# Optimization experiments

Measured on AMD Instinct MI355X. Metric: run time of the kernel, lower is better.

## Reference

```python
import jax, jax.numpy as jnp
import numpy as np

B, L, D, H, F, NL = 112, 128, 768, 12, 3072, 3
E = D // H  # head dim = 64
BN_EPS = 1e-5


def _bn(x, gamma, beta):
    # torch BatchNorm1d applied on x.permute(0,2,1): per-channel (d_model) stats over batch+seq
    mean = jnp.mean(x, axis=(0, 1), keepdims=True)
    var = jnp.var(x, axis=(0, 1), keepdims=True)
    return (x - mean) * jax.lax.rsqrt(var + BN_EPS) * gamma + beta


def setup_inputs() -> dict:
    key = jax.random.key(0)
    ks = jax.random.split(key, 10)
    s = 0.02
    inp = {
        "x": jax.random.normal(ks[0], (B, L, D), jnp.float32),
        "attn_bias": jax.random.normal(ks[1], (B, L, L, H), jnp.float32) * 0.1,
        "Wq": jax.random.normal(ks[2], (NL, D, D), jnp.float32) * s,
        "bq": jnp.zeros((NL, D), jnp.float32),
        "Wk": jax.random.normal(ks[3], (NL, D, D), jnp.float32) * s,
        "bk": jnp.zeros((NL, D), jnp.float32),
        "Wv": jax.random.normal(ks[4], (NL, D, D), jnp.float32) * s,
        "bv": jnp.zeros((NL, D), jnp.float32),
        "Wo": jax.random.normal(ks[5], (NL, D, D), jnp.float32) * s,
        "bo": jnp.zeros((NL, D), jnp.float32),
        "W1": jax.random.normal(ks[6], (NL, F, D), jnp.float32) * s,  # conv1 k=1 == Linear
        "b1": jnp.zeros((NL, F), jnp.float32),
        "W2": jax.random.normal(ks[7], (NL, D, F), jnp.float32) * s,  # conv2 k=1 == Linear
        "b2": jnp.zeros((NL, D), jnp.float32),
        "g1": jnp.ones((NL, D), jnp.float32),
        "be1": jnp.zeros((NL, D), jnp.float32),
        "g2": jnp.ones((NL, D), jnp.float32),
        "be2": jnp.zeros((NL, D), jnp.float32),
        "gf": jnp.ones((D,), jnp.float32),
        "bef": jnp.zeros((D,), jnp.float32),
    }
    return inp


def reference(x, attn_bias, Wq, bq, Wk, bk, Wv, bv, Wo, bo,
              W1, b1, W2, b2, g1, be1, g2, be2, gf, bef):
    scale = 1.0 / float(np.sqrt(E))
    bias_bhls = jnp.transpose(attn_bias, (0, 3, 1, 2))  # [B,H,L,S]
    for l in range(NL):
        q = (x @ Wq[l].T + bq[l]).reshape(B, L, H, E)
        k = (x @ Wk[l].T + bk[l]).reshape(B, L, H, E)
        v = (x @ Wv[l].T + bv[l]).reshape(B, L, H, E)
        scores = jnp.einsum('blhe,bshe->bhls', q, k)  # O(L^2) score tensor
        A = jax.nn.softmax(scores * scale + bias_bhls, axis=-1)
        V = jnp.einsum('bhls,bshd->blhd', A, v).reshape(B, L, D)
        new_x = V @ Wo[l].T + bo[l]
        x = _bn(x + new_x, g1[l], be1[l])
        y = jax.nn.gelu(x @ W1[l].T + b1[l], approximate=False)
        y = y @ W2[l].T + b2[l]
        x = _bn(x + y, g2[l], be2[l])
    return _bn(x, gf, bef)  # Encoder final BatchNorm1d(d_model)
```

## Files before the change

kernel.cpp:

```cpp
#include <hip/hip_runtime.h>

#define NB 112
#define SEQ 128
#define DM 768
#define NH 12
#define HD 64
#define FF 3072
#define NLAYER 3
#define MTOK (NB*SEQ)
#define QKVN (3*DM)
#define HEADTOT (NB*NH)
#define QSZ ((size_t)HEADTOT*SEQ*HD)

typedef unsigned short u16;
typedef __attribute__((ext_vector_type(8))) short short8;
typedef __attribute__((ext_vector_type(4))) float f32x4;
typedef __attribute__((ext_vector_type(4))) unsigned short us4;

__device__ __forceinline__ u16 f2bf(float f){
  unsigned u = __builtin_bit_cast(unsigned, f);
  u += 0x7FFFu + ((u >> 16) & 1u);
  return (u16)(u >> 16);
}
__device__ __forceinline__ float bf2f(u16 b){
  unsigned u = ((unsigned)b) << 16;
  return __builtin_bit_cast(float, u);
}
__device__ __forceinline__ unsigned cvt_pk_bf16(float lo, float hi){
  unsigned r;
  asm("v_cvt_pk_bf16_f32 %0, %1, %2" : "=v"(r) : "v"(lo), "v"(hi));
  return r;
}
__device__ __forceinline__ float gelu_t(float x){
  const float t = -1.5957691216057308f * x * __builtin_fmaf(0.044715f, x*x, 1.0f);
  return __fdividef(x, 1.0f + __expf(t));
}

__device__ __forceinline__ void gl_lds16(const void* g, void* l){
  __builtin_amdgcn_global_load_lds((const __attribute__((address_space(1))) unsigned*)g,
                                   (__attribute__((address_space(3))) unsigned*)l, 16, 0, 0);
}

template<int EPI>
__global__ __launch_bounds__(512, 2)
void gemm_bt(const u16* __restrict__ A, const u16* __restrict__ W,
             const float* __restrict__ bias, u16* __restrict__ obf,
             float* __restrict__ of32, const u16* __restrict__ res,
             float* __restrict__ p1, float* __restrict__ p2,
             int M, int N, int K, int Nt, int TPB)
{
  __shared__ __align__(16) char smem[131072];
  const int tid = threadIdx.x;
  const int w = tid >> 6, lane = tid & 63;
  const int wm = w >> 2, wn = w & 3;
  const int fr = lane & 15, fg = lane >> 4;
  const int fko = fg * 8;
  const int grid = gridDim.x;
  const int q8 = grid >> 3, r8 = grid & 7;
  const int xcd = blockIdx.x & 7, pos = blockIdx.x >> 3;
  const int start = xcd < r8 ? xcd * (q8 + 1) : r8 * (q8 + 1) + (xcd - r8) * q8;
  const int swz = start + pos;
  const int nt = K >> 6;
  const int tot = TPB * nt;
  const int l3 = lane >> 3;
  const int k16s = ((lane & 7) ^ l3) * 8;
  int rowAK[2][2], rowBK[2][2];
  #pragma unroll
  for (int mh = 0; mh < 2; mh++)
    #pragma unroll
    for (int j = 0; j < 2; j++)
      rowAK[mh][j] = (mh*64 + j*128 + w*8 + l3) * K;
  #pragma unroll
  for (int h = 0; h < 2; h++)
    #pragma unroll
    for (int j = 0; j < 2; j++)
      rowBK[h][j] = (h*128 + (w + j*8)*8 + l3) * K;

  auto stA2 = [&](int bb, int mh, int soff) {
    const u16* g0 = A + (size_t)soff + rowAK[mh][0] + k16s;
    const u16* g1 = A + (size_t)soff + rowAK[mh][1] + k16s;
    char* d = smem + bb*65536 + (mh*64 + w*8)*128;
    gl_lds16(g0, d);
    gl_lds16(g1, d + 16384);
  };
  auto stB2 = [&](int bb, int h, int soff) {
    const u16* g0 = W + (size_t)soff + rowBK[h][0] + k16s;
    const u16* g1 = W + (size_t)soff + rowBK[h][1] + k16s;
    char* d = smem + bb*65536 + 32768 + (h*128 + w*8)*128;
    gl_lds16(g0, d);
    gl_lds16(g1, d + 8192);
  };
  const int axor = (fr & 7) << 4;
  auto rdA2 = [&](int bb, int mh, int kh, int mf) -> short8 {
    const int row = wm*128 + mh*64 + mf*16 + fr;
    return *(const short8*)(smem + bb*65536 + row*128 + (((kh*32 + fko)*2) ^ axor));
  };
  auto rdB2 = [&](int bb, int kh, int nf) -> short8 {
    const int row = wn*64 + nf*16 + fr;
    return *(const short8*)(smem + bb*65536 + 32768 + row*128 + (((kh*32 + fko)*2) ^ axor));
  };
  auto coord = [&](int r, int& bm, int& bn) {
    const int lin = swz * TPB + r;
    const int mI = lin / Nt;
    bm = mI * 256; bn = (lin - mI * Nt) * 256;
  };

  f32x4 acc[8][4] = {};

  auto epi = [&](int bm, int bn) {
    float bs[4] = {0,0,0,0}, bq[4] = {0,0,0,0};
    #pragma unroll
    for (int mi = 0; mi < 8; mi++) {
      #pragma unroll
      for (int ni = 0; ni < 4; ni++) {
        const int c = bn + wn*64 + ni*16 + fr;
        const int r0 = bm + wm*128 + (mi>>2)*64 + (mi&3)*16 + fg*4;
        const float bc = bias[c];
        float v[4];
        #pragma unroll
        for (int j = 0; j < 4; j++) v[j] = acc[mi][ni][j] + bc;
        if constexpr (EPI == 1) {
          #pragma unroll
          for (int j = 0; j < 4; j++) v[j] = gelu_t(v[j]);
          const unsigned p01 = cvt_pk_bf16(v[0], v[1]);
          const unsigned p23 = cvt_pk_bf16(v[2], v[3]);
          u16* d = obf + (size_t)r0 * N + c;
          d[0] = (u16)p01; d[N] = (u16)(p01 >> 16);
          d[2*N] = (u16)p23; d[3*N] = (u16)(p23 >> 16);
        } else if constexpr (EPI == 2) {
          #pragma unroll
          for (int j = 0; j < 4; j++) {
            const float y = v[j] + bf2f(res[(size_t)(r0+j) * N + c]);
            of32[(size_t)(r0+j) * N + c] = y;
            bs[ni] += y; bq[ni] += y * y;
          }
        } else {
          const int which = c / DM;
          const int cc = c - which * DM;
          const int hh = cc >> 6, e = cc & 63;
          const int bb = r0 >> 7, l = r0 & 127;
          const unsigned p01 = cvt_pk_bf16(v[0], v[1]);
          const unsigned p23 = cvt_pk_bf16(v[2], v[3]);
          u16* d = obf + (size_t)which * QSZ + ((size_t)(bb*NH + hh) * SEQ + l) * HD + e;
          d[0] = (u16)p01; d[HD] = (u16)(p01 >> 16);
          d[2*HD] = (u16)p23; d[3*HD] = (u16)(p23 >> 16);
        }
        acc[mi][ni] = (f32x4){0.f, 0.f, 0.f, 0.f};
      }
    }
    if constexpr (EPI == 2) {
      const int mIdx = bm >> 8;
      #pragma unroll
      for (int ni = 0; ni < 4; ni++) {
        float s = bs[ni], qq = bq[ni];
        s  += __shfl_xor(s, 16);  s  += __shfl_xor(s, 32);
        qq += __shfl_xor(qq, 16); qq += __shfl_xor(qq, 32);
        if (fg == 0) {
          const int c = bn + wn*64 + ni*16 + fr;
          p1[(mIdx*2 + wm) * N + c] = s;
          p2[(mIdx*2 + wm) * N + c] = qq;
        }
      }
    }
  };

  int r0 = 0, kt0 = 0, bm0, bn0; coord(0, bm0, bn0);
  int r1 = 0, kt1 = 1, bm1 = bm0, bn1 = bn0;
  int r2 = 0, kt2 = 2, bm2 = bm0;
  if (kt2 >= nt) { kt2 -= nt; r2 = 1; int d; if (r2 < TPB) coord(r2, bm2, d); }

  stA2(0, 0, bm0*K); stA2(0, 1, bm0*K);
  stB2(0, 0, bn0*K); stB2(0, 1, bn0*K);
  if (tot > 1) stA2(1, 0, bm1*K + kt1*64);
  asm volatile("s_waitcnt vmcnt(2)" ::: "memory");
  __builtin_amdgcn_s_barrier();

  short8 bk0[4], bk1[4], av[4];
  for (int it = 0; it < tot; ++it) {
    const int bufc = it & 1, nb = bufc ^ 1;
    const bool st1 = (it + 1 < tot), st2 = (it + 2 < tot);
    const int sB1 = bn1*K + kt1*64;
    const int sA1 = bm1*K + kt1*64;
    const int sA2 = bm2*K + kt2*64;
    #pragma unroll
    for (int i = 0; i < 4; i++) av[i] = rdA2(bufc, 0, 0, i);
    #pragma unroll
    for (int i = 0; i < 4; i++) bk0[i] = rdB2(bufc, 0, i);
    if (st1) stB2(nb, 0, sB1);
    __builtin_amdgcn_s_barrier();
    asm volatile("s_waitcnt lgkmcnt(0)" ::: "memory");
    __builtin_amdgcn_sched_barrier(0);
    __builtin_amdgcn_s_setprio(1);
    #pragma unroll
    for (int mi = 0; mi < 4; mi++)
      #pragma unroll
      for (int ni = 0; ni < 4; ni++)
        acc[mi][ni] = __builtin_amdgcn_mfma_f32_16x16x32_bf16(av[mi], bk0[ni], acc[mi][ni], 0, 0, 0);
    __builtin_amdgcn_s_setprio(0);
    __builtin_amdgcn_s_barrier();
    #pragma unroll
    for (int i = 0; i < 4; i++) av[i] = rdA2(bufc, 0, 1, i);
    #pragma unroll
    for (int i = 0; i < 4; i++) bk1[i] = rdB2(bufc, 1, i);
    if (st1) stB2(nb, 1, sB1);
    __builtin_amdgcn_s_barrier();
    asm volatile("s_waitcnt lgkmcnt(0)" ::: "memory");
    __builtin_amdgcn_sched_barrier(0);
    __builtin_amdgcn_s_setprio(1);
    #pragma unroll
    for (int mi = 0; mi < 4; mi++)
      #pragma unroll
      for (int ni = 0; ni < 4; ni++)
        acc[mi][ni] = __builtin_amdgcn_mfma_f32_16x16x32_bf16(av[mi], bk1[ni], acc[mi][ni], 0, 0, 0);
    __builtin_amdgcn_s_setprio(0);
    if (st1) { asm volatile("s_waitcnt vmcnt(4)" ::: "memory"); }
    else     { asm volatile("s_waitcnt vmcnt(0)" ::: "memory"); }
    __builtin_amdgcn_s_barrier();
    #pragma unroll
    for (int i = 0; i < 4; i++) av[i] = rdA2(bufc, 1, 0, i);
    if (st2) stA2(bufc, 0, sA2);
    __builtin_amdgcn_s_barrier();
    asm volatile("s_waitcnt lgkmcnt(0)" ::: "memory");
    __builtin_amdgcn_sched_barrier(0);
    __builtin_amdgcn_s_setprio(1);
    #pragma unroll
    for (int mi = 0; mi < 4; mi++)
      #pragma unroll
      for (int ni = 0; ni < 4; ni++)
        acc[4+mi][ni] = __builtin_amdgcn_mfma_f32_16x16x32_bf16(av[mi], bk0[ni], acc[4+mi][ni], 0, 0, 0);
    __builtin_amdgcn_s_setprio(0);
    __builtin_amdgcn_s_barrier();
    #pragma unroll
    for (int i = 0; i < 4; i++) av[i] = rdA2(bufc, 1, 1, i);
    if (st1) stA2(nb, 1, sA1);
    __builtin_amdgcn_s_barrier();
    asm volatile("s_waitcnt lgkmcnt(0)" ::: "memory");
    __builtin_amdgcn_sched_barrier(0);
    __builtin_amdgcn_s_setprio(1);
    #pragma unroll
    for (int mi = 0; mi < 4; mi++)
      #pragma unroll
      for (int ni = 0; ni < 4; ni++)
        acc[4+mi][ni] = __builtin_amdgcn_mfma_f32_16x16x32_bf16(av[mi], bk1[ni], acc[4+mi][ni], 0, 0, 0);
    __builtin_amdgcn_s_setprio(0);
    if (st2)      { asm volatile("s_waitcnt vmcnt(4)" ::: "memory"); }
    else if (st1) { asm volatile("s_waitcnt vmcnt(2)" ::: "memory"); }
    __builtin_amdgcn_s_barrier();
    if (kt0 == nt - 1) {
      epi(bm0, bn0);
      kt0 = 0; r0++;
      if (r0 < TPB) coord(r0, bm0, bn0);
    } else kt0++;
    kt1++; if (kt1 == nt) { kt1 = 0; r1++; if (r1 < TPB) coord(r1, bm1, bn1); }
    kt2++; if (kt2 == nt) { kt2 = 0; r2++; if (r2 < TPB) { int d; coord(r2, bm2, d); } }
  }
}

__global__ __launch_bounds__(256)
void attn_kernel(const u16* __restrict__ qkvb, const u16* __restrict__ biasT,
                 u16* __restrict__ ab)
{
  const int h = blockIdx.x, b = blockIdx.y;
  const int tid = threadIdx.x, w = tid >> 6, lane = tid & 63;
  const int bh = b * NH + h;
  const u16* qp = qkvb + (size_t)bh * SEQ * HD;
  const u16* kp = qkvb + QSZ + (size_t)bh * SEQ * HD;
  const u16* vp = qkvb + 2 * QSZ + (size_t)bh * SEQ * HD;
  __shared__ __align__(16) u16 vT[HD * 136];
  __shared__ __align__(16) u16 P[SEQ * 136];
  {
    const int s = tid & 127, half = tid >> 7;
    #pragma unroll
    for (int rr = 0; rr < 4; rr++) {
      const int e0 = half * 32 + rr * 8;
      short8 v8 = *(const short8*)&vp[s * HD + e0];
      #pragma unroll
      for (int j = 0; j < 8; j++) vT[(e0 + j) * 136 + s] = (u16)v8[j];
    }
  }
  const int fr = lane & 15, fg = lane >> 4;
  f32x4 sacc[2][8] = {};
  #pragma unroll
  for (int ks = 0; ks < 2; ks++) {
    const int k0 = ks * 32 + fg * 8;
    short8 qf[2], kf[8];
    #pragma unroll
    for (int mi = 0; mi < 2; mi++) qf[mi] = *(const short8*)&qp[(w*32 + mi*16 + fr) * HD + k0];
    #pragma unroll
    for (int ni = 0; ni < 8; ni++) kf[ni] = *(const short8*)&kp[(ni*16 + fr) * HD + k0];
    #pragma unroll
    for (int mi = 0; mi < 2; mi++)
      #pragma unroll
      for (int ni = 0; ni < 8; ni++)
        sacc[mi][ni] = __builtin_amdgcn_mfma_f32_16x16x32_bf16(qf[mi], kf[ni], sacc[mi][ni], 0, 0, 0);
  }
  const u16* bt = biasT + (size_t)bh * SEQ * SEQ;
  #pragma unroll
  for (int mi = 0; mi < 2; mi++) {
    #pragma unroll
    for (int j = 0; j < 4; j++) {
      const int l = w*32 + mi*16 + fg*4 + j;
      float vals[8];
      float mx = -1e30f;
      #pragma unroll
      for (int ni = 0; ni < 8; ni++) {
        vals[ni] = sacc[mi][ni][j] * 0.125f + bf2f(bt[l * SEQ + ni*16 + fr]);
        mx = fmaxf(mx, vals[ni]);
      }
      #pragma unroll
      for (int d = 1; d < 16; d <<= 1) mx = fmaxf(mx, __shfl_xor(mx, d));
      float sum = 0.f;
      #pragma unroll
      for (int ni = 0; ni < 8; ni++) { vals[ni] = __expf(vals[ni] - mx); sum += vals[ni]; }
      #pragma unroll
      for (int d = 1; d < 16; d <<= 1) sum += __shfl_xor(sum, d);
      const float inv = 1.0f / sum;
      #pragma unroll
      for (int ni = 0; ni < 8; ni++) P[l * 136 + ni*16 + fr] = f2bf(vals[ni] * inv);
    }
  }
  __syncthreads();
  f32x4 oacc[2][4] = {};
  #pragma unroll
  for (int ss = 0; ss < 4; ss++) {
    const int s0 = ss * 32 + fg * 8;
    short8 pf[2], vf[4];
    #pragma unroll
    for (int mi = 0; mi < 2; mi++) pf[mi] = *(const short8*)&P[(w*32 + mi*16 + fr) * 136 + s0];
    #pragma unroll
    for (int ei = 0; ei < 4; ei++) vf[ei] = *(const short8*)&vT[(ei*16 + fr) * 136 + s0];
    #pragma unroll
    for (int mi = 0; mi < 2; mi++)
      #pragma unroll
      for (int ei = 0; ei < 4; ei++)
        oacc[mi][ei] = __builtin_amdgcn_mfma_f32_16x16x32_bf16(pf[mi], vf[ei], oacc[mi][ei], 0, 0, 0);
  }
  #pragma unroll
  for (int mi = 0; mi < 2; mi++)
    #pragma unroll
    for (int ei = 0; ei < 4; ei++)
      #pragma unroll
      for (int j = 0; j < 4; j++) {
        const int r = b * SEQ + w*32 + mi*16 + fg*4 + j;
        const int c = h * HD + ei*16 + fr;
        ab[(size_t)r * DM + c] = f2bf(oacc[mi][ei][j]);
      }
}

template<bool FINAL>
__global__ __launch_bounds__(256)
void bn_final(const float* __restrict__ p1, const float* __restrict__ p2,
              const float* __restrict__ ga, const float* __restrict__ be,
              const float* __restrict__ gb, const float* __restrict__ beb,
              float* __restrict__ sc, float* __restrict__ sh)
{
  const int c = blockIdx.x * 256 + threadIdx.x;
  float s = 0, q = 0;
  for (int i = 0; i < 112; i++) { s += p1[i * DM + c]; q += p2[i * DM + c]; }
  const float mean = s * (1.0f / MTOK);
  const float var = q * (1.0f / MTOK) - mean * mean;
  const float rstd = rsqrtf(var + 1e-5f);
  if constexpr (!FINAL) {
    const float g = ga[c] * rstd;
    sc[c] = g;
    sh[c] = be[c] - mean * g;
  } else {
    const float sc2 = ga[c] * rstd;
    const float sh2 = be[c] - mean * sc2;
    const float varf = sc2 * sc2 * var;
    const float meanf = sc2 * mean + sh2;
    const float scf = gb[c] * rsqrtf(varf + 1e-5f);
    const float shf = beb[c] - meanf * scf;
    sc[c] = scf * sc2;
    sh[c] = scf * sh2 + shf;
  }
}

template<int MODE>
__global__ __launch_bounds__(256)
void bn_apply(const float* __restrict__ xi, const float* __restrict__ sc,
              const float* __restrict__ sh, float* __restrict__ xo, u16* __restrict__ xb)
{
  const int i = blockIdx.x * 256 + threadIdx.x;
  const int cv = i % (DM / 4);
  float4 v = ((const float4*)xi)[i];
  const float4 s = ((const float4*)sc)[cv];
  const float4 h = ((const float4*)sh)[cv];
  float4 y;
  y.x = v.x * s.x + h.x; y.y = v.y * s.y + h.y;
  y.z = v.z * s.z + h.z; y.w = v.w * s.w + h.w;
  if constexpr (MODE == 1) {
    ((float4*)xo)[i] = y;
  } else {
    us4 pk; pk[0] = f2bf(y.x); pk[1] = f2bf(y.y); pk[2] = f2bf(y.z); pk[3] = f2bf(y.w);
    *(us4*)(xb + (size_t)i * 4) = pk;
  }
}

__global__ __launch_bounds__(256)
void conv_bf16(const float* __restrict__ s, u16* __restrict__ d, int n4)
{
  const int i = blockIdx.x * 256 + threadIdx.x;
  if (i >= n4) return;
  float4 v = ((const float4*)s)[i];
  us4 pk; pk[0] = f2bf(v.x); pk[1] = f2bf(v.y); pk[2] = f2bf(v.z); pk[3] = f2bf(v.w);
  *(us4*)(d + (size_t)i * 4) = pk;
}

__global__ __launch_bounds__(256)
void conv_qkvw(const float* __restrict__ wq, const float* __restrict__ wk,
               const float* __restrict__ wv, u16* __restrict__ d)
{
  const int i = blockIdx.x * 256 + threadIdx.x;
  const int per = QKVN * DM / 4;
  const int l = i / per;
  const int rem = i - l * per;
  const int r = rem / (DM / 4);
  const int cv = rem - r * (DM / 4);
  const float* srcrow;
  if (r < DM)          srcrow = wq + ((size_t)l * DM + r) * DM;
  else if (r < 2 * DM) srcrow = wk + ((size_t)l * DM + (r - DM)) * DM;
  else                 srcrow = wv + ((size_t)l * DM + (r - 2 * DM)) * DM;
  float4 v = ((const float4*)srcrow)[cv];
  us4 pk; pk[0] = f2bf(v.x); pk[1] = f2bf(v.y); pk[2] = f2bf(v.z); pk[3] = f2bf(v.w);
  *(us4*)(d + (size_t)i * 4) = pk;
}

__global__ __launch_bounds__(256)
void conv_bias_qkv(const float* __restrict__ bq, const float* __restrict__ bk,
                   const float* __restrict__ bv, float* __restrict__ d)
{
  const int i = blockIdx.x * 256 + threadIdx.x;
  const int l = i / QKVN;
  const int r = i - l * QKVN;
  float v;
  if (r < DM)          v = bq[l * DM + r];
  else if (r < 2 * DM) v = bk[l * DM + r - DM];
  else                 v = bv[l * DM + r - 2 * DM];
  d[i] = v;
}

__global__ __launch_bounds__(256)
void bias_tr(const float* __restrict__ src, u16* __restrict__ dst)
{
  const int l = blockIdx.x, b = blockIdx.y;
  __shared__ float row[SEQ * NH];
  const float* s = src + ((size_t)b * SEQ + l) * SEQ * NH;
  for (int i = threadIdx.x; i < SEQ * NH; i += 256) row[i] = s[i];
  __syncthreads();
  for (int i = threadIdx.x; i < SEQ * NH; i += 256) {
    const int h = i >> 7, ss = i & 127;
    dst[((size_t)(b * NH + h) * SEQ + l) * SEQ + ss] = f2bf(row[ss * NH + h]);
  }
}

extern "C" void kernel_launch(void* const* d_in, const int* in_sizes, int n_in,
                              void* d_out, int out_size, void* d_ws, size_t ws_size,
                              hipStream_t stream)
{
  const float* x    = (const float*)d_in[0];
  const float* abia = (const float*)d_in[1];
  const float* Wq   = (const float*)d_in[2];
  const float* bq   = (const float*)d_in[3];
  const float* Wk   = (const float*)d_in[4];
  const float* bk   = (const float*)d_in[5];
  const float* Wv   = (const float*)d_in[6];
  const float* bv   = (const float*)d_in[7];
  const float* Wo   = (const float*)d_in[8];
  const float* bo   = (const float*)d_in[9];
  const float* W1   = (const float*)d_in[10];
  const float* b1   = (const float*)d_in[11];
  const float* W2   = (const float*)d_in[12];
  const float* b2   = (const float*)d_in[13];
  const float* g1   = (const float*)d_in[14];
  const float* be1  = (const float*)d_in[15];
  const float* g2   = (const float*)d_in[16];
  const float* be2  = (const float*)d_in[17];
  const float* gf   = (const float*)d_in[18];
  const float* bef  = (const float*)d_in[19];
  float* out = (float*)d_out;

  char* ws = (char*)d_ws;
  size_t off = 0;
  auto alloc = [&](size_t n) -> char* {
    char* p = ws + off;
    off = (off + n + 255) & ~(size_t)255;
    return p;
  };
  u16*  wqkv  = (u16*)alloc((size_t)3 * QKVN * DM * 2);
  u16*  wo    = (u16*)alloc((size_t)3 * DM * DM * 2);
  u16*  w1    = (u16*)alloc((size_t)3 * FF * DM * 2);
  u16*  w2    = (u16*)alloc((size_t)3 * DM * FF * 2);
  float* bqkv = (float*)alloc((size_t)3 * QKVN * 4);
  u16*  xb    = (u16*)alloc((size_t)MTOK * DM * 2);
  u16*  ab    = (u16*)alloc((size_t)MTOK * DM * 2);
  u16*  big   = (u16*)alloc((size_t)MTOK * FF * 2);
  u16*  biasT = (u16*)alloc((size_t)HEADTOT * SEQ * SEQ * 2);
  float* p1   = (float*)alloc((size_t)112 * DM * 4);
  float* p2   = (float*)alloc((size_t)112 * DM * 4);
  float* sc   = (float*)alloc(DM * 4);
  float* sh   = (float*)alloc(DM * 4);
  if (off > ws_size) return;

  conv_qkvw<<<5184, 256, 0, stream>>>(Wq, Wk, Wv, wqkv);
  conv_bf16<<<1728, 256, 0, stream>>>(Wo, wo, 3 * DM * DM / 4);
  conv_bf16<<<6912, 256, 0, stream>>>(W1, w1, 3 * FF * DM / 4);
  conv_bf16<<<6912, 256, 0, stream>>>(W2, w2, 3 * DM * FF / 4);
  conv_bias_qkv<<<27, 256, 0, stream>>>(bq, bk, bv, bqkv);
  bias_tr<<<dim3(SEQ, NB), 256, 0, stream>>>(abia, biasT);
  conv_bf16<<<MTOK * DM / 4 / 256, 256, 0, stream>>>(x, xb, MTOK * DM / 4);

  auto gemm = [&](int epi, const u16* Ap, const u16* Wp, const float* bp,
                  u16* ob, float* o32, const u16* rs, int M, int N, int K) {
    const int Nt = N / 256;
    const int tiles = (M / 256) * Nt;
    const int tpb = (tiles + 255) / 256;
    const int grid = tiles / tpb;
    if (epi == 1)
      gemm_bt<1><<<grid, 512, 0, stream>>>(Ap, Wp, bp, ob, o32, rs, p1, p2, M, N, K, Nt, tpb);
    else if (epi == 2)
      gemm_bt<2><<<grid, 512, 0, stream>>>(Ap, Wp, bp, ob, o32, rs, p1, p2, M, N, K, Nt, tpb);
    else
      gemm_bt<3><<<grid, 512, 0, stream>>>(Ap, Wp, bp, ob, o32, rs, p1, p2, M, N, K, Nt, tpb);
  };

  for (int l = 0; l < NLAYER; l++) {
    gemm(3, xb, wqkv + (size_t)l * QKVN * DM, bqkv + l * QKVN, big, nullptr, nullptr,
         MTOK, QKVN, DM);
    attn_kernel<<<dim3(NH, NB), 256, 0, stream>>>(big, biasT, ab);
    gemm(2, ab, wo + (size_t)l * DM * DM, bo + l * DM, nullptr, out, xb,
         MTOK, DM, DM);
    bn_final<false><<<3, 256, 0, stream>>>(p1, p2, g1 + l * DM, be1 + l * DM,
                                           nullptr, nullptr, sc, sh);
    bn_apply<0><<<MTOK * DM / 4 / 256, 256, 0, stream>>>(out, sc, sh, nullptr, xb);
    gemm(1, xb, w1 + (size_t)l * FF * DM, b1 + l * FF, big, nullptr, nullptr,
         MTOK, FF, DM);
    gemm(2, big, w2 + (size_t)l * DM * FF, b2 + l * DM, nullptr, out, xb,
         MTOK, DM, FF);
    if (l < NLAYER - 1) {
      bn_final<false><<<3, 256, 0, stream>>>(p1, p2, g2 + l * DM, be2 + l * DM,
                                             nullptr, nullptr, sc, sh);
      bn_apply<0><<<MTOK * DM / 4 / 256, 256, 0, stream>>>(out, sc, sh, nullptr, xb);
    } else {
      bn_final<true><<<3, 256, 0, stream>>>(p1, p2, g2 + l * DM, be2 + l * DM,
                                            gf, bef, sc, sh);
      bn_apply<1><<<MTOK * DM / 4 / 256, 256, 0, stream>>>(out, sc, sh, out, nullptr);
    }
  }
}
```

Baseline: 1.172 ms.

## Fold BatchNorm affine into following GEMM weights and residual epilogues

Drops the standalone bn_apply passes between layers. The BatchNorm scale is folded into the next GEMM's weight columns (scale_w), and the shift is folded into its bias (fold_bias). The residual epilogue applies the affine to the un-normalized residual, and outputs stay in bf16 (pre-BN) rather than fp32. The epilogue is also split into two halves interleaved with the final k-step, to overlap stores with MFMA work. This saves full-activation read/write passes, at the cost of small per-layer weight rescale kernels and bf16 rounding of pre-normalized activations and scaled weights.

```diff
diff --git a/kernel.cpp b/kernel.cpp
--- a/kernel.cpp
+++ b/kernel.cpp
@@ -46,6 +46,7 @@
 void gemm_bt(const u16* __restrict__ A, const u16* __restrict__ W,
              const float* __restrict__ bias, u16* __restrict__ obf,
              float* __restrict__ of32, const u16* __restrict__ res,
+             const float* __restrict__ rsc, const float* __restrict__ rsh,
              float* __restrict__ p1, float* __restrict__ p2,
              int M, int N, int K, int Nt, int TPB)
 {
@@ -107,15 +108,17 @@
 
   f32x4 acc[8][4] = {};
 
-  auto epi = [&](int bm, int bn) {
-    float bs[4] = {0,0,0,0}, bq[4] = {0,0,0,0};
-    #pragma unroll
-    for (int mi = 0; mi < 8; mi++) {
-      #pragma unroll
-      for (int ni = 0; ni < 4; ni++) {
-        const int c = bn + wn*64 + ni*16 + fr;
-        const int r0 = bm + wm*128 + (mi>>2)*64 + (mi&3)*16 + fg*4;
-        const float bc = bias[c];
+  auto epih = [&](int half, int bm, int bn, float* bsp, float* bqp) {
+    #pragma unroll
+    for (int ni = 0; ni < 4; ni++) {
+      const int c = bn + wn*64 + ni*16 + fr;
+      const float bc = bias[c];
+      float rs = 0.f, rh = 0.f;
+      if constexpr (EPI == 2 || EPI == 4) { rs = rsc[c]; rh = rsh[c]; }
+      #pragma unroll
+      for (int mq = 0; mq < 4; mq++) {
+        const int mi = half*4 + mq;
+        const int r0 = bm + wm*128 + half*64 + mq*16 + fg*4;
         float v[4];
         #pragma unroll
         for (int j = 0; j < 4; j++) v[j] = acc[mi][ni][j] + bc;
@@ -127,12 +130,14 @@
           u16* d = obf + (size_t)r0 * N + c;
           d[0] = (u16)p01; d[N] = (u16)(p01 >> 16);
           d[2*N] = (u16)p23; d[3*N] = (u16)(p23 >> 16);
-        } else if constexpr (EPI == 2) {
+        } else if constexpr (EPI == 2 || EPI == 4) {
           #pragma unroll
           for (int j = 0; j < 4; j++) {
-            const float y = v[j] + bf2f(res[(size_t)(r0+j) * N + c]);
-            of32[(size_t)(r0+j) * N + c] = y;
-            bs[ni] += y; bq[ni] += y * y;
+            const float rv = bf2f(res[(size_t)(r0+j) * N + c]);
+            const float y = v[j] + __builtin_fmaf(rs, rv, rh);
+            if constexpr (EPI == 4) of32[(size_t)(r0+j) * N + c] = y;
+            else                    obf[(size_t)(r0+j) * N + c] = f2bf(y);
+            bsp[ni] += y; bqp[ni] += y * y;
           }
         } else {
           const int which = c / DM;
@@ -148,23 +153,9 @@
         acc[mi][ni] = (f32x4){0.f, 0.f, 0.f, 0.f};
       }
     }
-    if constexpr (EPI == 2) {
-      const int mIdx = bm >> 8;
-      #pragma unroll
-      for (int ni = 0; ni < 4; ni++) {
-        float s = bs[ni], qq = bq[ni];
-        s  += __shfl_xor(s, 16);  s  += __shfl_xor(s, 32);
-        qq += __shfl_xor(qq, 16); qq += __shfl_xor(qq, 32);
-        if (fg == 0) {
-          const int c = bn + wn*64 + ni*16 + fr;
-          p1[(mIdx*2 + wm) * N + c] = s;
-          p2[(mIdx*2 + wm) * N + c] = qq;
-        }
-      }
-    }
-  };
-
-  int r0 = 0, kt0 = 0, bm0, bn0; coord(0, bm0, bn0);
+  };
+
+  int r0t = 0, kt0 = 0, bm0, bn0; coord(0, bm0, bn0);
   int r1 = 0, kt1 = 1, bm1 = bm0, bn1 = bn0;
   int r2 = 0, kt2 = 2, bm2 = bm0;
   if (kt2 >= nt) { kt2 -= nt; r2 = 1; int d; if (r2 < TPB) coord(r2, bm2, d); }
@@ -179,6 +170,8 @@
   for (int it = 0; it < tot; ++it) {
     const int bufc = it & 1, nb = bufc ^ 1;
     const bool st1 = (it + 1 < tot), st2 = (it + 2 < tot);
+    const bool last = (kt0 == nt - 1);
+    float bs[4] = {0,0,0,0}, bq[4] = {0,0,0,0};
     const int sB1 = bn1*K + kt1*64;
     const int sA1 = bm1*K + kt1*64;
     const int sA2 = bm2*K + kt2*64;
@@ -216,6 +209,7 @@
     if (st1) { asm volatile("s_waitcnt vmcnt(4)" ::: "memory"); }
     else     { asm volatile("s_waitcnt vmcnt(0)" ::: "memory"); }
     __builtin_amdgcn_s_barrier();
+    if (last) epih(0, bm0, bn0, bs, bq);
     #pragma unroll
     for (int i = 0; i < 4; i++) av[i] = rdA2(bufc, 1, 0, i);
     if (st2) stA2(bufc, 0, sA2);
@@ -246,10 +240,24 @@
     if (st2)      { asm volatile("s_waitcnt vmcnt(4)" ::: "memory"); }
     else if (st1) { asm volatile("s_waitcnt vmcnt(2)" ::: "memory"); }
     __builtin_amdgcn_s_barrier();
-    if (kt0 == nt - 1) {
-      epi(bm0, bn0);
-      kt0 = 0; r0++;
-      if (r0 < TPB) coord(r0, bm0, bn0);
+    if (last) {
+      epih(1, bm0, bn0, bs, bq);
+      if constexpr (EPI == 2 || EPI == 4) {
+        const int mIdx = bm0 >> 8;
+        #pragma unroll
+        for (int ni = 0; ni < 4; ni++) {
+          float s = bs[ni], qq = bq[ni];
+          s  += __shfl_xor(s, 16);  s  += __shfl_xor(s, 32);
+          qq += __shfl_xor(qq, 16); qq += __shfl_xor(qq, 32);
+          if (fg == 0) {
+            const int c = bn0 + wn*64 + ni*16 + fr;
+            p1[(mIdx*2 + wm) * N + c] = s;
+            p2[(mIdx*2 + wm) * N + c] = qq;
+          }
+        }
+      }
+      kt0 = 0; r0t++;
+      if (r0t < TPB) coord(r0t, bm0, bn0);
     } else kt0++;
     kt1++; if (kt1 == nt) { kt1 = 0; r1++; if (r1 < TPB) coord(r1, bm1, bn1); }
     kt2++; if (kt2 == nt) { kt2 = 0; r2++; if (r2 < TPB) { int d; coord(r2, bm2, d); } }
@@ -376,10 +384,9 @@
   }
 }
 
-template<int MODE>
-__global__ __launch_bounds__(256)
-void bn_apply(const float* __restrict__ xi, const float* __restrict__ sc,
-              const float* __restrict__ sh, float* __restrict__ xo, u16* __restrict__ xb)
+__global__ __launch_bounds__(256)
+void bn_apply_f32(const float* __restrict__ xi, const float* __restrict__ sc,
+                  const float* __restrict__ sh, float* __restrict__ xo)
 {
   const int i = blockIdx.x * 256 + threadIdx.x;
   const int cv = i % (DM / 4);
@@ -389,12 +396,51 @@
   float4 y;
   y.x = v.x * s.x + h.x; y.y = v.y * s.y + h.y;
   y.z = v.z * s.z + h.z; y.w = v.w * s.w + h.w;
-  if constexpr (MODE == 1) {
-    ((float4*)xo)[i] = y;
-  } else {
-    us4 pk; pk[0] = f2bf(y.x); pk[1] = f2bf(y.y); pk[2] = f2bf(y.z); pk[3] = f2bf(y.w);
-    *(us4*)(xb + (size_t)i * 4) = pk;
-  }
+  ((float4*)xo)[i] = y;
+}
+
+__global__ __launch_bounds__(256)
+void scale_w(const u16* __restrict__ w, const float* __restrict__ sc,
+             u16* __restrict__ d, int total8, int K)
+{
+  const int i = blockIdx.x * 256 + threadIdx.x;
+  if (i >= total8) return;
+  const int base = i * 8;
+  const int col = base % K;
+  short8 v = *(const short8*)&w[base];
+  const float4 s0 = *(const float4*)&sc[col];
+  const float4 s1 = *(const float4*)&sc[col + 4];
+  short8 r;
+  r[0] = (short)f2bf(bf2f((u16)v[0]) * s0.x);
+  r[1] = (short)f2bf(bf2f((u16)v[1]) * s0.y);
+  r[2] = (short)f2bf(bf2f((u16)v[2]) * s0.z);
+  r[3] = (short)f2bf(bf2f((u16)v[3]) * s0.w);
+  r[4] = (short)f2bf(bf2f((u16)v[4]) * s1.x);
+  r[5] = (short)f2bf(bf2f((u16)v[5]) * s1.y);
+  r[6] = (short)f2bf(bf2f((u16)v[6]) * s1.z);
+  r[7] = (short)f2bf(bf2f((u16)v[7]) * s1.w);
+  *(short8*)&d[base] = r;
+}
+
+__global__ __launch_bounds__(256)
+void fold_bias(const u16* __restrict__ w, const float* __restrict__ sh,
+               const float* __restrict__ b, float* __restrict__ bout, int N, int K)
+{
+  const int n = blockIdx.x * 4 + (threadIdx.x >> 6);
+  const int lane = threadIdx.x & 63;
+  if (n >= N) return;
+  float s = 0.f;
+  for (int k = lane; k < K; k += 64) s += bf2f(w[(size_t)n * K + k]) * sh[k];
+  #pragma unroll
+  for (int d = 1; d < 64; d <<= 1) s += __shfl_xor(s, d);
+  if (lane == 0) bout[n] = b[n] + s;
+}
+
+__global__ __launch_bounds__(256)
+void init_affine(float* __restrict__ one, float* __restrict__ zero)
+{
+  const int i = blockIdx.x * 256 + threadIdx.x;
+  if (i < DM) { one[i] = 1.0f; zero[i] = 0.0f; }
 }
 
 __global__ __launch_bounds__(256)
@@ -493,13 +539,22 @@
   u16*  w2    = (u16*)alloc((size_t)3 * DM * FF * 2);
   float* bqkv = (float*)alloc((size_t)3 * QKVN * 4);
   u16*  xb    = (u16*)alloc((size_t)MTOK * DM * 2);
+  u16*  xc    = (u16*)alloc((size_t)MTOK * DM * 2);
   u16*  ab    = (u16*)alloc((size_t)MTOK * DM * 2);
   u16*  big   = (u16*)alloc((size_t)MTOK * FF * 2);
   u16*  biasT = (u16*)alloc((size_t)HEADTOT * SEQ * SEQ * 2);
+  u16*  wqs   = (u16*)alloc((size_t)QKVN * DM * 2);
+  u16*  w1s   = (u16*)alloc((size_t)FF * DM * 2);
+  float* bqs  = (float*)alloc(QKVN * 4);
+  float* b1s  = (float*)alloc(FF * 4);
   float* p1   = (float*)alloc((size_t)112 * DM * 4);
   float* p2   = (float*)alloc((size_t)112 * DM * 4);
-  float* sc   = (float*)alloc(DM * 4);
-  float* sh   = (float*)alloc(DM * 4);
+  float* sc1  = (float*)alloc(DM * 4);
+  float* sh1  = (float*)alloc(DM * 4);
+  float* scP  = (float*)alloc(DM * 4);
+  float* shP  = (float*)alloc(DM * 4);
+  float* id1  = (float*)alloc(DM * 4);
+  float* id0  = (float*)alloc(DM * 4);
   if (off > ws_size) return;
 
   conv_qkvw<<<5184, 256, 0, stream>>>(Wq, Wk, Wv, wqkv);
@@ -509,42 +564,57 @@
   conv_bias_qkv<<<27, 256, 0, stream>>>(bq, bk, bv, bqkv);
   bias_tr<<<dim3(SEQ, NB), 256, 0, stream>>>(abia, biasT);
   conv_bf16<<<MTOK * DM / 4 / 256, 256, 0, stream>>>(x, xb, MTOK * DM / 4);
+  init_affine<<<3, 256, 0, stream>>>(id1, id0);
 
   auto gemm = [&](int epi, const u16* Ap, const u16* Wp, const float* bp,
-                  u16* ob, float* o32, const u16* rs, int M, int N, int K) {
+                  u16* ob, float* o32, const u16* rs, const float* rscp,
+                  const float* rshp, int M, int N, int K) {
     const int Nt = N / 256;
     const int tiles = (M / 256) * Nt;
     const int tpb = (tiles + 255) / 256;
     const int grid = tiles / tpb;
     if (epi == 1)
-      gemm_bt<1><<<grid, 512, 0, stream>>>(Ap, Wp, bp, ob, o32, rs, p1, p2, M, N, K, Nt, tpb);
+      gemm_bt<1><<<grid, 512, 0, stream>>>(Ap, Wp, bp, ob, o32, rs, rscp, rshp, p1, p2, M, N, K, Nt, tpb);
     else if (epi == 2)
-      gemm_bt<2><<<grid, 512, 0, stream>>>(Ap, Wp, bp, ob, o32, rs, p1, p2, M, N, K, Nt, tpb);
+      gemm_bt<2><<<grid, 512, 0, stream>>>(Ap, Wp, bp, ob, o32, rs, rscp, rshp, p1, p2, M, N, K, Nt, tpb);
+    else if (epi == 3)
+      gemm_bt<3><<<grid, 512, 0, stream>>>(Ap, Wp, bp, ob, o32, rs, rscp, rshp, p1, p2, M, N, K, Nt, tpb);
     else
-      gemm_bt<3><<<grid, 512, 0, stream>>>(Ap, Wp, bp, ob, o32, rs, p1, p2, M, N, K, Nt, tpb);
-  };
+      gemm_bt<4><<<grid, 512, 0, stream>>>(Ap, Wp, bp, ob, o32, rs, rscp, rshp, p1, p2, M, N, K, Nt, tpb);
+  };
+
+  const float* scIn = id1;
+  const float* shIn = id0;
 
   for (int l = 0; l < NLAYER; l++) {
-    gemm(3, xb, wqkv + (size_t)l * QKVN * DM, bqkv + l * QKVN, big, nullptr, nullptr,
-         MTOK, QKVN, DM);
+    const u16* wqe; const float* bqe;
+    if (l == 0) { wqe = wqkv; bqe = bqkv; }
+    else {
+      scale_w<<<(QKVN*DM/8 + 255)/256, 256, 0, stream>>>(wqkv + (size_t)l*QKVN*DM, scIn, wqs, QKVN*DM/8, DM);
+      fold_bias<<<QKVN/4, 256, 0, stream>>>(wqkv + (size_t)l*QKVN*DM, shIn, bqkv + l*QKVN, bqs, QKVN, DM);
+      wqe = wqs; bqe = bqs;
+    }
+    gemm(3, xb, wqe, bqe, big, nullptr, nullptr, nullptr, nullptr, MTOK, QKVN, DM);
     attn_kernel<<<dim3(NH, NB), 256, 0, stream>>>(big, biasT, ab);
-    gemm(2, ab, wo + (size_t)l * DM * DM, bo + l * DM, nullptr, out, xb,
+    gemm(2, ab, wo + (size_t)l * DM * DM, bo + l * DM, xc, nullptr, xb, scIn, shIn,
          MTOK, DM, DM);
     bn_final<false><<<3, 256, 0, stream>>>(p1, p2, g1 + l * DM, be1 + l * DM,
-                                           nullptr, nullptr, sc, sh);
-    bn_apply<0><<<MTOK * DM / 4 / 256, 256, 0, stream>>>(out, sc, sh, nullptr, xb);
-    gemm(1, xb, w1 + (size_t)l * FF * DM, b1 + l * FF, big, nullptr, nullptr,
-         MTOK, FF, DM);
-    gemm(2, big, w2 + (size_t)l * DM * FF, b2 + l * DM, nullptr, out, xb,
-         MTOK, DM, FF);
+                                           nullptr, nullptr, sc1, sh1);
+    scale_w<<<(FF*DM/8 + 255)/256, 256, 0, stream>>>(w1 + (size_t)l*FF*DM, sc1, w1s, FF*DM/8, DM);
+    fold_bias<<<FF/4, 256, 0, stream>>>(w1 + (size_t)l*FF*DM, sh1, b1 + l*FF, b1s, FF, DM);
+    gemm(1, xc, w1s, b1s, big, nullptr, nullptr, nullptr, nullptr, MTOK, FF, DM);
     if (l < NLAYER - 1) {
+      gemm(2, big, w2 + (size_t)l * DM * FF, b2 + l * DM, xb, nullptr, xc, sc1, sh1,
+           MTOK, DM, FF);
       bn_final<false><<<3, 256, 0, stream>>>(p1, p2, g2 + l * DM, be2 + l * DM,
-                                             nullptr, nullptr, sc, sh);
-      bn_apply<0><<<MTOK * DM / 4 / 256, 256, 0, stream>>>(out, sc, sh, nullptr, xb);
+                                             nullptr, nullptr, scP, shP);
+      scIn = scP; shIn = shP;
     } else {
+      gemm(4, big, w2 + (size_t)l * DM * FF, b2 + l * DM, nullptr, out, xc, sc1, sh1,
+           MTOK, DM, FF);
       bn_final<true><<<3, 256, 0, stream>>>(p1, p2, g2 + l * DM, be2 + l * DM,
-                                            gf, bef, sc, sh);
-      bn_apply<1><<<MTOK * DM / 4 / 256, 256, 0, stream>>>(out, sc, sh, out, nullptr);
+                                            gf, bef, sc1, sh1);
+      bn_apply_f32<<<MTOK * DM / 4 / 256, 256, 0, stream>>>(out, sc1, sh1, out);
     }
   }
 }
```

Measured after the change: 1.392 ms. 1.19x slower.
